# Kernel optimization log

Measured on AMD Instinct MI355X. Metric: run time of the kernel, lower is better.

Reference implementation:

```python
import jax, jax.numpy as jnp
import numpy as np

# Dims: C = 8*8*4 = 256 input channels, O = 8*8*8 = 512 output channels,
# space_rank = 4, TT ranks = (4, 16, 16).

def setup_inputs() -> dict:
    key = jax.random.key(0)
    ks = jax.random.split(key, 6)
    inp = jax.random.normal(ks[0], (32, 256, 32, 32), dtype=jnp.float32)
    # space_factor: (space_rank, 1, kH, kW)
    space_factor = jax.random.normal(ks[1], (4, 1, 3, 3), dtype=jnp.float32) * 0.3
    # factors[i]: (in_i, rank_i, rank_{i+1}, out_i)
    factor0 = jax.random.normal(ks[2], (8, 4, 16, 8), dtype=jnp.float32) * 0.1
    factor1 = jax.random.normal(ks[3], (8, 16, 16, 8), dtype=jnp.float32) * 0.08
    # last_factor: (in_last, rank_last, out_last)
    last_factor = jax.random.normal(ks[4], (4, 16, 8), dtype=jnp.float32) * 0.1
    bias = jax.random.uniform(ks[5], (512,), dtype=jnp.float32, minval=-0.02, maxval=0.02)
    return {"input": inp, "space_factor": space_factor, "factor0": factor0,
            "factor1": factor1, "last_factor": last_factor, "bias": bias}


def reference(input, space_factor, factor0, factor1, last_factor, bias):
    B, C, H, W = input.shape
    sr = space_factor.shape[0]
    # Depthwise conv: each of the C channels convolved with the same
    # `space_rank` filters (torch repeat along out-channel dim + groups=C).
    w = jnp.tile(space_factor, (C, 1, 1, 1))  # (C*sr, 1, kH, kW)
    y = jax.lax.conv_general_dilated(
        input, w, window_strides=(1, 1), padding=[(1, 1), (1, 1)],
        feature_group_count=C,
        dimension_numbers=("NCHW", "OIHW", "NCHW"))  # (B, C*sr, H', W')
    Hp, Wp = y.shape[2], y.shape[3]
    # (B, n0, n1, n2, sr, H', W') with (n0,n1,n2) = input_chanel_shape
    t = y.reshape(B, 8, 8, 4, sr, Hp, Wp)
    # Contract the tiny TT cores first (optimal order found by tn.contractors.optimal):
    # chain: (n0, n1, n2, r0, o0, o1, o2) -- only ~0.5M elements.
    chain = jnp.einsum("apqx,bqry,crz->abcpxyz", factor0, factor1, last_factor)
    # One big contraction over (n0, n1, n2, r0): effectively a GEMM
    # (B*H'*W', C*sr) x (C*sr, O).
    out = jnp.einsum("nabcphw,abcpxyz->nxyzhw", t, chain)
    out = out.reshape(B, 512, Hp, Wp)
    return out + bias[None, :, None, None]
```

## Files before the change

kernel.cpp:

```cpp
#include <hip/hip_runtime.h>

typedef unsigned short ushort_t;
typedef __attribute__((ext_vector_type(8))) short bf16x8;
typedef __attribute__((ext_vector_type(8))) unsigned short ushort8;
typedef __attribute__((ext_vector_type(4))) float f32x4;

__device__ __forceinline__ unsigned short f2bf(float f) {
  union { float f; unsigned u; } x; x.f = f;
  unsigned r = x.u + 0x7FFFu + ((x.u >> 16) & 1u);
  return (unsigned short)(r >> 16);
}

__global__ __launch_bounds__(256) void chain_kernel(const float* __restrict__ f0,
                                                    const float* __restrict__ f1,
                                                    const float* __restrict__ lf,
                                                    ushort_t* __restrict__ chainT) {
  __shared__ float gs[512];
  int o = blockIdx.x;
  int z = o & 7, y = (o >> 3) & 7, x = o >> 6;
  int tid = threadIdx.x;
  #pragma unroll
  for (int i = 0; i < 2; ++i) {
    int e = tid + i * 256;
    int c = e & 3, q = (e >> 2) & 15, b = e >> 6;
    float s = 0.f;
    #pragma unroll
    for (int r = 0; r < 16; ++r)
      s += f1[((b * 16 + q) * 16 + r) * 8 + y] * lf[(c * 16 + r) * 8 + z];
    gs[e] = s;
  }
  __syncthreads();
  #pragma unroll
  for (int j = 0; j < 4; ++j) {
    int k = tid + j * 256;
    int p = k & 3, c = (k >> 2) & 3, b = (k >> 4) & 7, a = k >> 7;
    float s = 0.f;
    #pragma unroll
    for (int q = 0; q < 16; ++q)
      s += f0[((a * 4 + p) * 16 + q) * 8 + x] * gs[(b * 16 + q) * 4 + c];
    chainT[(size_t)o * 1024 + k] = f2bf(s);
  }
}

__global__ __launch_bounds__(256) void conv_kernel(const float* __restrict__ in,
                                                   const float* __restrict__ sf,
                                                   ushort_t* __restrict__ t) {
  __shared__ float in_lds[16][404];
  __shared__ float sf_l[36];
  int bid = blockIdx.x;
  int cg = bid & 15, hg = (bid >> 4) & 3, n = bid >> 6;
  int h0 = hg * 8;
  int tid = threadIdx.x;
  if (tid < 36) sf_l[tid] = sf[tid];
  for (int e = tid; e < 320; e += 256) {
    int ch = e / 20, rr = e % 20;
    in_lds[ch][(rr >> 1) * 40 + 3 + (rr & 1) * 33] = 0.f;
  }
  const float* inb = in + ((size_t)n * 256 + cg * 16) * 1024;
  #pragma unroll
  for (int i = 0; i < 5; ++i) {
    int e = tid + i * 256;
    int ch = e / 80, rem = e % 80;
    int r = rem >> 3, w4 = rem & 7;
    int hh = h0 - 1 + r;
    float4 v = make_float4(0.f, 0.f, 0.f, 0.f);
    if (hh >= 0 && hh < 32)
      v = *(const float4*)&inb[(size_t)ch * 1024 + hh * 32 + w4 * 4];
    *(float4*)&in_lds[ch][r * 40 + 4 + w4 * 4] = v;
  }
  __syncthreads();
  float sfr[36];
  #pragma unroll
  for (int i = 0; i < 36; ++i) sfr[i] = sf_l[i];
  int w = tid & 31, sub = tid >> 5;
  size_t m0 = (size_t)n * 1024 + (size_t)h0 * 32 + w;
  unsigned pw[8][4];
  #pragma unroll
  for (int b = 0; b < 2; ++b) {
    int ch = sub * 2 + b;
    float vals[10][3];
    #pragma unroll
    for (int r = 0; r < 10; ++r)
      #pragma unroll
      for (int dw = 0; dw < 3; ++dw)
        vals[r][dw] = in_lds[ch][r * 40 + 3 + w + dw];
    #pragma unroll
    for (int j = 0; j < 8; ++j) {
      float s0 = 0.f, s1 = 0.f, s2 = 0.f, s3 = 0.f;
      #pragma unroll
      for (int dr = 0; dr < 3; ++dr)
        #pragma unroll
        for (int dw = 0; dw < 3; ++dw) {
          float tv = vals[j + dr][dw];
          s0 += tv * sfr[0 * 9 + dr * 3 + dw];
          s1 += tv * sfr[1 * 9 + dr * 3 + dw];
          s2 += tv * sfr[2 * 9 + dr * 3 + dw];
          s3 += tv * sfr[3 * 9 + dr * 3 + dw];
        }
      pw[j][b * 2 + 0] = (unsigned)f2bf(s0) | ((unsigned)f2bf(s1) << 16);
      pw[j][b * 2 + 1] = (unsigned)f2bf(s2) | ((unsigned)f2bf(s3) << 16);
    }
  }
  #pragma unroll
  for (int j = 0; j < 8; ++j) {
    uint4 pk; pk.x = pw[j][0]; pk.y = pw[j][1]; pk.z = pw[j][2]; pk.w = pw[j][3];
    *(uint4*)&t[(m0 + (size_t)j * 32) * 1024 + (size_t)(cg * 64 + sub * 8)] = pk;
  }
}

#define AS1 __attribute__((address_space(1)))
#define AS3 __attribute__((address_space(3)))
#define BARRIER  __builtin_amdgcn_s_barrier()
#define LGKMCNT0 asm volatile("s_waitcnt lgkmcnt(0)" ::: "memory")
#define VMCNT2   asm volatile("s_waitcnt vmcnt(2)" ::: "memory")
#define VMCNT0   asm volatile("s_waitcnt vmcnt(0)" ::: "memory")

__global__ __launch_bounds__(512, 4) void gemm_kernel(const ushort_t* __restrict__ tA,
                                                      const ushort_t* __restrict__ tB,
                                                      const float* __restrict__ bias,
                                                      float* __restrict__ out) {
  __shared__ __align__(16) ushort_t smem[32768];
  int tid = threadIdx.x;
  int bid = blockIdx.x;
  int wg = (bid & 7) * 128 + (bid >> 3);
  int tile_m = (wg >> 2) * 128;
  int tile_n = (wg & 3) * 128;

  int lane = tid & 63, wv = tid >> 6;
  int wm = (wv >> 1) * 32, wn = (wv & 1) * 64;
  int lr = lane & 15, kg = lane >> 4;
  int kph0 = ((kg * 8) ^ ((lane & 7) * 8));
  int kph1 = ((32 + kg * 8) ^ ((lane & 7) * 8));
  int arow = wm + lr;
  int brow = wn + lr;

  int srow = tid >> 3;
  int scol = ((tid & 7) ^ (srow & 7)) * 8;
  const ushort_t* sA = tA + (size_t)(tile_m + srow) * 1024 + scol;
  const ushort_t* sB = tB + (size_t)(tile_n + srow) * 1024 + scol;

#define STAGE_A(buf, koff, h)                                                                  \
  __builtin_amdgcn_global_load_lds((const AS1 void*)(sA + (size_t)((h)*64) * 1024 + (koff)),   \
      (AS3 void*)&smem[(buf)*8192 + (h)*4096 + tid*8], 16, 0, 0);
#define STAGE_B(buf, koff, h)                                                                  \
  __builtin_amdgcn_global_load_lds((const AS1 void*)(sB + (size_t)((h)*64) * 1024 + (koff)),   \
      (AS3 void*)&smem[16384 + (buf)*8192 + (h)*4096 + tid*8], 16, 0, 0);

#define READ_A1(dst, buf)                                                                      \
  dst[0] = *(const bf16x8*)&smem[(buf)*8192 + (arow)*64 + kph0];                               \
  dst[1] = *(const bf16x8*)&smem[(buf)*8192 + (arow)*64 + kph1];
#define READ_A2(dst, buf)                                                                      \
  dst[0] = *(const bf16x8*)&smem[(buf)*8192 + (arow + 16)*64 + kph0];                          \
  dst[1] = *(const bf16x8*)&smem[(buf)*8192 + (arow + 16)*64 + kph1];
#define READ_B(dst, nbase, buf)                                                                \
  _Pragma("unroll")                                                                            \
  for (int nf = 0; nf < 2; ++nf) {                                                             \
    dst[nf][0] = *(const bf16x8*)&smem[16384 + (buf)*8192 + (brow + (nbase) + nf*16)*64 + kph0];\
    dst[nf][1] = *(const bf16x8*)&smem[16384 + (buf)*8192 + (brow + (nbase) + nf*16)*64 + kph1];\
  }
#define Q_MFMA(AF, BF, MB, NB)                                                                 \
  __builtin_amdgcn_s_setprio(1);                                                              \
  _Pragma("unroll")                                                                            \
  for (int nf = 0; nf < 2; ++nf)                                                               \
    _Pragma("unroll")                                                                          \
    for (int ks = 0; ks < 2; ++ks)                                                             \
      acc[MB][(NB) + nf] = __builtin_amdgcn_mfma_f32_16x16x32_bf16(                            \
          AF[ks], BF[nf][ks], acc[MB][(NB) + nf], 0, 0, 0);                                    \
  __builtin_amdgcn_s_setprio(0);

  f32x4 acc[2][4];
  #pragma unroll
  for (int i = 0; i < 2; ++i)
    #pragma unroll
    for (int j = 0; j < 4; ++j) acc[i][j] = (f32x4){0.f, 0.f, 0.f, 0.f};

  bf16x8 a1[2], a2[2], b1[2][2], b2[2][2];

  STAGE_A(0, 0, 0) STAGE_A(0, 0, 1) STAGE_B(0, 0, 0) STAGE_B(0, 0, 1)
  STAGE_A(1, 64, 0) STAGE_A(1, 64, 1)
  VMCNT2; BARRIER;

#define ITER(I_, FULL)                                                                         \
  {                                                                                            \
    int k1 = (2*(I_)+1)*64, k2 = (2*(I_)+2)*64, k3 = (2*(I_)+3)*64;                            \
                                                 \
    READ_A1(a1, 0) READ_B(b1, 0, 0)                                                            \
    STAGE_B(1, k1, 0)                                                                          \
    Q_MFMA(a1, b1, 0, 0) BARRIER;                                                              \
                   \
    READ_B(b2, 32, 0) READ_A2(a2, 0)                                                           \
    STAGE_B(1, k1, 1)                                                                          \
    Q_MFMA(a1, b2, 0, 2) LGKMCNT0; BARRIER;                                                    \
                                                                 \
    if (FULL) { STAGE_A(0, k2, 0) }                                                            \
    Q_MFMA(a2, b2, 1, 2) BARRIER;                                                              \
                                                           \
    if (FULL) { STAGE_A(0, k2, 1) }                                                            \
    Q_MFMA(a2, b1, 1, 0)                                                                       \
    if (FULL) { VMCNT2; } else { VMCNT0; }                                                     \
    BARRIER;                                                                                   \
                                                                           \
    READ_A1(a1, 1) READ_B(b1, 0, 1)                                                            \
    if (FULL) { STAGE_B(0, k2, 0) }                                                            \
    Q_MFMA(a1, b1, 0, 0) BARRIER;                                                              \
                                                                                       \
    READ_B(b2, 32, 1) READ_A2(a2, 1)                                                           \
    if (FULL) { STAGE_B(0, k2, 1) }                                                            \
    Q_MFMA(a1, b2, 0, 2) LGKMCNT0; BARRIER;                                                    \
                                                                                       \
    if (FULL) { STAGE_A(1, k3, 0) }                                                            \
    Q_MFMA(a2, b2, 1, 2) BARRIER;                                                              \
                                                      \
    if (FULL) { STAGE_A(1, k3, 1) }                                                            \
    Q_MFMA(a2, b1, 1, 0)                                                                       \
    if (FULL) { VMCNT2; BARRIER; }                                                             \
  }

  for (int I = 0; I < 7; ++I) ITER(I, 1)
  ITER(7, 0)
#undef ITER

  #pragma unroll
  for (int mf = 0; mf < 2; ++mf)
    #pragma unroll
    for (int nf = 0; nf < 4; ++nf) {
      int m = tile_m + wm + mf * 16 + kg * 4;
      int o = tile_n + wn + nf * 16 + lr;
      float bv = bias[o];
      f32x4 v = acc[mf][nf];
      v[0] += bv; v[1] += bv; v[2] += bv; v[3] += bv;
      *(f32x4*)&out[(size_t)(m >> 10) * 524288 + (size_t)o * 1024 + (size_t)(m & 1023)] = v;
    }
}

extern "C" void kernel_launch(void* const* d_in, const int* in_sizes, int n_in,
                              void* d_out, int out_size, void* d_ws, size_t ws_size,
                              hipStream_t stream) {
  (void)in_sizes; (void)n_in; (void)out_size; (void)ws_size;
  const float* in   = (const float*)d_in[0];
  const float* sf   = (const float*)d_in[1];
  const float* f0   = (const float*)d_in[2];
  const float* f1   = (const float*)d_in[3];
  const float* lf   = (const float*)d_in[4];
  const float* bias = (const float*)d_in[5];
  float* out = (float*)d_out;

  char* ws = (char*)d_ws;
  ushort_t* t      = (ushort_t*)ws;
  ushort_t* chainT = (ushort_t*)(ws + 67108864);

  hipLaunchKernelGGL(chain_kernel, dim3(512),  dim3(256), 0, stream, f0, f1, lf, chainT);
  hipLaunchKernelGGL(conv_kernel,  dim3(2048), dim3(256), 0, stream, in, sf, t);
  hipLaunchKernelGGL(gemm_kernel,  dim3(1024), dim3(512), 0, stream, t, chainT, bias, out);
}
```

Measured before the change: 70.71 us.

## Use 4 waves per GEMM block with 64x64 per-wave tiles

The GEMM block shrinks from 512 to 256 threads. Each wave now computes a 64x64 output sub-tile (4x4 MFMA accumulators) instead of 32x64, which raises register-level reuse of the A and B fragments per LDS read. Each thread issues four global-to-LDS loads per stage instead of two, and the vmcnt waits are adjusted to match. The cost is more registers per wave and half as many waves per block to hide latency.

```diff
diff --git a/kernel.cpp b/kernel.cpp
--- a/kernel.cpp
+++ b/kernel.cpp
@@ -112,10 +112,10 @@
 #define AS3 __attribute__((address_space(3)))
 #define BARRIER  __builtin_amdgcn_s_barrier()
 #define LGKMCNT0 asm volatile("s_waitcnt lgkmcnt(0)" ::: "memory")
-#define VMCNT2   asm volatile("s_waitcnt vmcnt(2)" ::: "memory")
+#define VMCNT4   asm volatile("s_waitcnt vmcnt(4)" ::: "memory")
 #define VMCNT0   asm volatile("s_waitcnt vmcnt(0)" ::: "memory")
 
-__global__ __launch_bounds__(512, 4) void gemm_kernel(const ushort_t* __restrict__ tA,
+__global__ __launch_bounds__(256, 2) void gemm_kernel(const ushort_t* __restrict__ tA,
                                                       const ushort_t* __restrict__ tB,
                                                       const float* __restrict__ bias,
                                                       float* __restrict__ out) {
@@ -127,7 +127,7 @@
   int tile_n = (wg & 3) * 128;
 
   int lane = tid & 63, wv = tid >> 6;
-  int wm = (wv >> 1) * 32, wn = (wv & 1) * 64;
+  int wm = (wv >> 1) * 64, wn = (wv & 1) * 64;
   int lr = lane & 15, kg = lane >> 4;
   int kph0 = ((kg * 8) ^ ((lane & 7) * 8));
   int kph1 = ((32 + kg * 8) ^ ((lane & 7) * 8));
@@ -139,81 +139,96 @@
   const ushort_t* sA = tA + (size_t)(tile_m + srow) * 1024 + scol;
   const ushort_t* sB = tB + (size_t)(tile_n + srow) * 1024 + scol;
 
-#define STAGE_A(buf, koff, h)                                                                  \
-  __builtin_amdgcn_global_load_lds((const AS1 void*)(sA + (size_t)((h)*64) * 1024 + (koff)),   \
-      (AS3 void*)&smem[(buf)*8192 + (h)*4096 + tid*8], 16, 0, 0);
-#define STAGE_B(buf, koff, h)                                                                  \
-  __builtin_amdgcn_global_load_lds((const AS1 void*)(sB + (size_t)((h)*64) * 1024 + (koff)),   \
-      (AS3 void*)&smem[16384 + (buf)*8192 + (h)*4096 + tid*8], 16, 0, 0);
+#define STAGE_A(buf, koff, q)                                                                  \
+  __builtin_amdgcn_global_load_lds((const AS1 void*)(sA + (size_t)((q)*32) * 1024 + (koff)),   \
+      (AS3 void*)&smem[(buf)*8192 + (q)*2048 + tid*8], 16, 0, 0);
+#define STAGE_B(buf, koff, q)                                                                  \
+  __builtin_amdgcn_global_load_lds((const AS1 void*)(sB + (size_t)((q)*32) * 1024 + (koff)),   \
+      (AS3 void*)&smem[16384 + (buf)*8192 + (q)*2048 + tid*8], 16, 0, 0);
 
 #define READ_A1(dst, buf)                                                                      \
-  dst[0] = *(const bf16x8*)&smem[(buf)*8192 + (arow)*64 + kph0];                               \
-  dst[1] = *(const bf16x8*)&smem[(buf)*8192 + (arow)*64 + kph1];
+  _Pragma("unroll")                                                                            \
+  for (int mf = 0; mf < 2; ++mf) {                                                             \
+    dst[mf][0] = *(const bf16x8*)&smem[(buf)*8192 + (arow + mf*16)*64 + kph0];                 \
+    dst[mf][1] = *(const bf16x8*)&smem[(buf)*8192 + (arow + mf*16)*64 + kph1];                 \
+  }
 #define READ_A2(dst, buf)                                                                      \
-  dst[0] = *(const bf16x8*)&smem[(buf)*8192 + (arow + 16)*64 + kph0];                          \
-  dst[1] = *(const bf16x8*)&smem[(buf)*8192 + (arow + 16)*64 + kph1];
-#define READ_B(dst, nbase, buf)                                                                \
+  _Pragma("unroll")                                                                            \
+  for (int mf = 0; mf < 2; ++mf) {                                                             \
+    dst[mf][0] = *(const bf16x8*)&smem[(buf)*8192 + (arow + 32 + mf*16)*64 + kph0];            \
+    dst[mf][1] = *(const bf16x8*)&smem[(buf)*8192 + (arow + 32 + mf*16)*64 + kph1];            \
+  }
+#define READ_B1(dst, buf)                                                                      \
   _Pragma("unroll")                                                                            \
   for (int nf = 0; nf < 2; ++nf) {                                                             \
-    dst[nf][0] = *(const bf16x8*)&smem[16384 + (buf)*8192 + (brow + (nbase) + nf*16)*64 + kph0];\
-    dst[nf][1] = *(const bf16x8*)&smem[16384 + (buf)*8192 + (brow + (nbase) + nf*16)*64 + kph1];\
+    dst[nf][0] = *(const bf16x8*)&smem[16384 + (buf)*8192 + (brow + nf*16)*64 + kph0];         \
+    dst[nf][1] = *(const bf16x8*)&smem[16384 + (buf)*8192 + (brow + nf*16)*64 + kph1];         \
+  }
+#define READ_B2(dst, buf)                                                                      \
+  _Pragma("unroll")                                                                            \
+  for (int nf = 0; nf < 2; ++nf) {                                                             \
+    dst[nf][0] = *(const bf16x8*)&smem[16384 + (buf)*8192 + (brow + 32 + nf*16)*64 + kph0];    \
+    dst[nf][1] = *(const bf16x8*)&smem[16384 + (buf)*8192 + (brow + 32 + nf*16)*64 + kph1];    \
   }
 #define Q_MFMA(AF, BF, MB, NB)                                                                 \
   __builtin_amdgcn_s_setprio(1);                                                              \
   _Pragma("unroll")                                                                            \
-  for (int nf = 0; nf < 2; ++nf)                                                               \
+  for (int mf = 0; mf < 2; ++mf)                                                               \
     _Pragma("unroll")                                                                          \
-    for (int ks = 0; ks < 2; ++ks)                                                             \
-      acc[MB][(NB) + nf] = __builtin_amdgcn_mfma_f32_16x16x32_bf16(                            \
-          AF[ks], BF[nf][ks], acc[MB][(NB) + nf], 0, 0, 0);                                    \
+    for (int nf = 0; nf < 2; ++nf)                                                             \
+      _Pragma("unroll")                                                                        \
+      for (int ks = 0; ks < 2; ++ks)                                                           \
+        acc[(MB) + mf][(NB) + nf] = __builtin_amdgcn_mfma_f32_16x16x32_bf16(                   \
+            AF[mf][ks], BF[nf][ks], acc[(MB) + mf][(NB) + nf], 0, 0, 0);                       \
   __builtin_amdgcn_s_setprio(0);
 
-  f32x4 acc[2][4];
-  #pragma unroll
-  for (int i = 0; i < 2; ++i)
+  f32x4 acc[4][4];
+  #pragma unroll
+  for (int i = 0; i < 4; ++i)
     #pragma unroll
     for (int j = 0; j < 4; ++j) acc[i][j] = (f32x4){0.f, 0.f, 0.f, 0.f};
 
-  bf16x8 a1[2], a2[2], b1[2][2], b2[2][2];
-
-  STAGE_A(0, 0, 0) STAGE_A(0, 0, 1) STAGE_B(0, 0, 0) STAGE_B(0, 0, 1)
-  STAGE_A(1, 64, 0) STAGE_A(1, 64, 1)
-  VMCNT2; BARRIER;
+  bf16x8 a1[2][2], a2[2][2], b1[2][2], b2[2][2];
+
+  STAGE_A(0, 0, 0) STAGE_A(0, 0, 1) STAGE_A(0, 0, 2) STAGE_A(0, 0, 3)
+  STAGE_B(0, 0, 0) STAGE_B(0, 0, 1) STAGE_B(0, 0, 2) STAGE_B(0, 0, 3)
+  STAGE_A(1, 64, 0) STAGE_A(1, 64, 1) STAGE_A(1, 64, 2) STAGE_A(1, 64, 3)
+  VMCNT4; BARRIER;
 
 #define ITER(I_, FULL)                                                                         \
   {                                                                                            \
     int k1 = (2*(I_)+1)*64, k2 = (2*(I_)+2)*64, k3 = (2*(I_)+3)*64;                            \
                                                  \
-    READ_A1(a1, 0) READ_B(b1, 0, 0)                                                            \
-    STAGE_B(1, k1, 0)                                                                          \
+    READ_A1(a1, 0) READ_B1(b1, 0)                                                              \
+    STAGE_B(1, k1, 0) STAGE_B(1, k1, 1)                                                        \
     Q_MFMA(a1, b1, 0, 0) BARRIER;                                                              \
                    \
-    READ_B(b2, 32, 0) READ_A2(a2, 0)                                                           \
-    STAGE_B(1, k1, 1)                                                                          \
+    READ_B2(b2, 0) READ_A2(a2, 0)                                                              \
+    STAGE_B(1, k1, 2) STAGE_B(1, k1, 3)                                                        \
     Q_MFMA(a1, b2, 0, 2) LGKMCNT0; BARRIER;                                                    \
                                                                  \
-    if (FULL) { STAGE_A(0, k2, 0) }                                                            \
-    Q_MFMA(a2, b2, 1, 2) BARRIER;                                                              \
+    if (FULL) { STAGE_A(0, k2, 0) STAGE_A(0, k2, 1) }                                          \
+    Q_MFMA(a2, b2, 2, 2) BARRIER;                                                              \
                                                            \
-    if (FULL) { STAGE_A(0, k2, 1) }                                                            \
-    Q_MFMA(a2, b1, 1, 0)                                                                       \
-    if (FULL) { VMCNT2; } else { VMCNT0; }                                                     \
+    if (FULL) { STAGE_A(0, k2, 2) STAGE_A(0, k2, 3) }                                          \
+    Q_MFMA(a2, b1, 2, 0)                                                                       \
+    if (FULL) { VMCNT4; } else { VMCNT0; }                                                     \
     BARRIER;                                                                                   \
                                                                            \
-    READ_A1(a1, 1) READ_B(b1, 0, 1)                                                            \
-    if (FULL) { STAGE_B(0, k2, 0) }                                                            \
+    READ_A1(a1, 1) READ_B1(b1, 1)                                                              \
+    if (FULL) { STAGE_B(0, k2, 0) STAGE_B(0, k2, 1) }                                          \
     Q_MFMA(a1, b1, 0, 0) BARRIER;                                                              \
                                                                                        \
-    READ_B(b2, 32, 1) READ_A2(a2, 1)                                                           \
-    if (FULL) { STAGE_B(0, k2, 1) }                                                            \
+    READ_B2(b2, 1) READ_A2(a2, 1)                                                              \
+    if (FULL) { STAGE_B(0, k2, 2) STAGE_B(0, k2, 3) }                                          \
     Q_MFMA(a1, b2, 0, 2) LGKMCNT0; BARRIER;                                                    \
                                                                                        \
-    if (FULL) { STAGE_A(1, k3, 0) }                                                            \
-    Q_MFMA(a2, b2, 1, 2) BARRIER;                                                              \
+    if (FULL) { STAGE_A(1, k3, 0) STAGE_A(1, k3, 1) }                                          \
+    Q_MFMA(a2, b2, 2, 2) BARRIER;                                                              \
                                                       \
-    if (FULL) { STAGE_A(1, k3, 1) }                                                            \
-    Q_MFMA(a2, b1, 1, 0)                                                                       \
-    if (FULL) { VMCNT2; BARRIER; }                                                             \
+    if (FULL) { STAGE_A(1, k3, 2) STAGE_A(1, k3, 3) }                                          \
+    Q_MFMA(a2, b1, 2, 0)                                                                       \
+    if (FULL) { VMCNT4; BARRIER; }                                                             \
   }
 
   for (int I = 0; I < 7; ++I) ITER(I, 1)
@@ -221,7 +236,7 @@
 #undef ITER
 
   #pragma unroll
-  for (int mf = 0; mf < 2; ++mf)
+  for (int mf = 0; mf < 4; ++mf)
     #pragma unroll
     for (int nf = 0; nf < 4; ++nf) {
       int m = tile_m + wm + mf * 16 + kg * 4;
@@ -251,5 +266,5 @@
 
   hipLaunchKernelGGL(chain_kernel, dim3(512),  dim3(256), 0, stream, f0, f1, lf, chainT);
   hipLaunchKernelGGL(conv_kernel,  dim3(2048), dim3(256), 0, stream, in, sf, t);
-  hipLaunchKernelGGL(gemm_kernel,  dim3(1024), dim3(512), 0, stream, t, chainT, bias, out);
-}
+  hipLaunchKernelGGL(gemm_kernel,  dim3(1024), dim3(256), 0, stream, t, chainT, bias, out);
+}
```

Result: faster. 69.22 us (-2.1%).
